# Performance work log

Measured on AMD Instinct MI355X. Metric: run time of the kernel, lower is better.

The kernel has to match this reference:

```python
import jax, jax.numpy as jnp
import numpy as np

EPS = 1e-5

def _bn(x, g, b):
    # BatchNorm2d in training mode: batch stats over (N,H,W), biased variance
    m = x.mean(axis=(0, 2, 3), keepdims=True)
    v = x.var(axis=(0, 2, 3), keepdims=True)
    return g[None, :, None, None] * (x - m) * jax.lax.rsqrt(v + EPS) + b[None, :, None, None]

def _conv(x, w, b, stride, pad):
    y = jax.lax.conv_general_dilated(x, w, (stride, stride), [(pad, pad), (pad, pad)],
                                     dimension_numbers=('NCHW', 'OIHW', 'NCHW'))
    return y + b[None, :, None, None]

def _convT(x, w, b):
    # torch ConvTranspose2d(k=4, s=2, p=1); w is torch layout (C_in, C_out, kH, kW)
    wt = jnp.flip(w, axis=(2, 3)).transpose(1, 0, 2, 3)  # -> OIHW
    y = jax.lax.conv_general_dilated(x, wt, (1, 1), [(2, 2), (2, 2)], lhs_dilation=(2, 2),
                                     dimension_numbers=('NCHW', 'OIHW', 'NCHW'))
    return y + b[None, :, None, None]

def setup_inputs() -> dict:
    key = jax.random.key(0)
    ks = jax.random.split(key, 20)
    K, C = 512, 64
    r = lambda k, sh, s=0.05: (jax.random.normal(k, sh, dtype=jnp.float32) * s)
    return {
        'x': jax.random.uniform(ks[0], (256, 1, 128, 128), dtype=jnp.float32),
        'enc_w1': r(ks[1], (16, 1, 4, 4)), 'enc_b1': r(ks[2], (16,)),
        'bn1_g': jnp.ones((16,), jnp.float32), 'bn1_b': jnp.zeros((16,), jnp.float32),
        'enc_w2': r(ks[3], (32, 16, 4, 4)), 'enc_b2': r(ks[4], (32,)),
        'bn2_g': jnp.ones((32,), jnp.float32), 'bn2_b': jnp.zeros((32,), jnp.float32),
        'enc_w3': r(ks[5], (64, 32, 1, 1)), 'enc_b3': r(ks[6], (64,)),
        'bn3_g': jnp.ones((64,), jnp.float32), 'bn3_b': jnp.zeros((64,), jnp.float32),
        'emb': jax.random.normal(ks[7], (K, C), dtype=jnp.float32) / K,
        'dec_w1': r(ks[8], (32, 64, 1, 1)), 'dec_b1': r(ks[9], (32,)),
        'bn4_g': jnp.ones((32,), jnp.float32), 'bn4_b': jnp.zeros((32,), jnp.float32),
        'dec_w2': r(ks[10], (32, 16, 4, 4)), 'dec_b2': r(ks[11], (16,)),  # ConvT torch layout (in,out,kh,kw)
        'bn5_g': jnp.ones((16,), jnp.float32), 'bn5_b': jnp.zeros((16,), jnp.float32),
        'dec_w3': r(ks[12], (16, 1, 4, 4)), 'dec_b3': r(ks[13], (1,)),
    }

def reference(x, enc_w1, enc_b1, bn1_g, bn1_b, enc_w2, enc_b2, bn2_g, bn2_b,
              enc_w3, enc_b3, bn3_g, bn3_b, emb,
              dec_w1, dec_b1, bn4_g, bn4_b, dec_w2, dec_b2, bn5_g, bn5_b,
              dec_w3, dec_b3):
    # ---- encoder ----
    h = jax.nn.relu(_bn(_conv(x, enc_w1, enc_b1, 2, 1), bn1_g, bn1_b))
    h = jax.nn.relu(_bn(_conv(h, enc_w2, enc_b2, 2, 1), bn2_g, bn2_b))
    z_e_x = _bn(_conv(h, enc_w3, enc_b3, 1, 0), bn3_g, bn3_b)  # [N,64,H/4,W/4]
    # ---- VQ: nearest codebook entry by squared L2 ----
    z = z_e_x.transpose(0, 2, 3, 1)  # NHWC
    dists = ((z * z).sum(-1, keepdims=True)
             - 2.0 * jnp.einsum('nhwc,kc->nhwk', z, emb)
             + (emb * emb).sum(-1))  # [N,H,W,K]
    latents = jnp.argmin(dists, axis=-1)
    z_q_x = emb[latents].transpose(0, 3, 1, 2)  # [N,64,H/4,W/4]
    # ---- decoder ----
    d = jax.nn.relu(_bn(_conv(z_q_x, dec_w1, dec_b1, 1, 0), bn4_g, bn4_b))
    d = jax.nn.relu(_bn(_convT(d, dec_w2, dec_b2), bn5_g, bn5_b))
    x_tilde = jax.nn.sigmoid(_convT(d, dec_w3, dec_b3))
    return (x_tilde, z_e_x, z_q_x)
```

## Files before the change

kernel.cpp:

```cpp
#include <hip/hip_runtime.h>

__device__ inline double wave_red(double v) {
#pragma unroll
  for (int off = 32; off > 0; off >>= 1) v += __shfl_down(v, off, 64);
  return v;
}
__device__ inline double block_red(double v, double* lds) {
  double w = wave_red(v);
  int lane = threadIdx.x & 63, wid = threadIdx.x >> 6;
  if (lane == 0) lds[wid] = w;
  __syncthreads();
  double r = 0.0;
  if (threadIdx.x == 0) r = (lds[0] + lds[1]) + (lds[2] + lds[3]);
  __syncthreads();
  return r;
}

__global__ __launch_bounds__(256) void conv1_k(const float* __restrict__ x, const float* __restrict__ w,
                                               const float* __restrict__ bias, float* __restrict__ y) {
  int t = blockIdx.x * 256 + threadIdx.x;
  int n = t >> 12, oh = (t >> 6) & 63, ow = t & 63;
  const float* xb = x + n * 16384;
  int ih0 = 2 * oh - 1, iw0 = 2 * ow - 1;
  float patch[16];
#pragma unroll
  for (int kh = 0; kh < 4; ++kh) {
    int ih = ih0 + kh;
    bool vh = (unsigned)ih < 128u;
#pragma unroll
    for (int kw = 0; kw < 4; ++kw) {
      int iw = iw0 + kw;
      patch[kh * 4 + kw] = (vh && (unsigned)iw < 128u) ? xb[ih * 128 + iw] : 0.f;
    }
  }
  float* yb = y + n * 65536 + oh * 64 + ow;
#pragma unroll
  for (int c = 0; c < 16; ++c) {
    float acc = 0.f;
#pragma unroll
    for (int q = 0; q < 16; ++q) acc = fmaf(patch[q], w[c * 16 + q], acc);
    yb[c * 4096] = __fadd_rn(acc, bias[c]);
  }
}

__global__ __launch_bounds__(256) void statsA_k(const float* __restrict__ y, double* __restrict__ ps,
                                                double* __restrict__ pq, int hwlog, int C, int M, int SPLIT) {
  int c = blockIdx.x, s = blockIdx.y;
  int HWm = (1 << hwlog) - 1;
  double sum = 0.0, sq = 0.0;
  for (int i = s * 256 + threadIdx.x; i < M; i += SPLIT * 256) {
    int n = i >> hwlog, hw = i & HWm;
    double v = (double)y[(size_t)n * (C << hwlog) + (c << hwlog) + hw];
    sum += v;
    sq = fma(v, v, sq);
  }
  __shared__ double lds[4];
  double S = block_red(sum, lds);
  double Q = block_red(sq, lds);
  if (threadIdx.x == 0) { ps[c * SPLIT + s] = S; pq[c * SPLIT + s] = Q; }
}

__global__ void finB_k(const double* __restrict__ ps, const double* __restrict__ pq,
                       float* __restrict__ ss, int C, int SPLIT, double invM) {
  int c = threadIdx.x;
  if (c >= C) return;
  double S = 0.0, Q = 0.0;
  for (int i = 0; i < SPLIT; ++i) { S += ps[c * SPLIT + i]; Q += pq[c * SPLIT + i]; }
  double mean = S * invM;
  float m32 = (float)mean;
  double v = Q * invM - 2.0 * (double)m32 * mean + (double)m32 * (double)m32;
  float v32 = (float)v;
  ss[c] = m32;
  ss[C + c] = 1.0f / sqrtf(__fadd_rn(v32, 1e-5f));
}

__global__ __launch_bounds__(256) void conv2_k(const float* __restrict__ y1, const float* __restrict__ ss,
                                               const float* __restrict__ w, const float* __restrict__ bias,
                                               float* __restrict__ y2) {
  int t = blockIdx.x * 256 + threadIdx.x;
  int n = t >> 10, oh = (t >> 5) & 31, ow = t & 31;
  const float* xb = y1 + n * 65536;
  int ih0 = 2 * oh - 1, iw0 = 2 * ow - 1;
  float acc[32];
#pragma unroll
  for (int co = 0; co < 32; ++co) acc[co] = 0.f;
  for (int ci = 0; ci < 16; ++ci) {
    float m = ss[ci], r = ss[16 + ci];
    const float* xc = xb + ci * 4096;
    float patch[16];
#pragma unroll
    for (int kh = 0; kh < 4; ++kh) {
      int ih = ih0 + kh;
      bool vh = (unsigned)ih < 64u;
#pragma unroll
      for (int kw = 0; kw < 4; ++kw) {
        int iw = iw0 + kw;
        float v = 0.f;
        if (vh && (unsigned)iw < 64u) v = fmaxf(__fmul_rn(__fsub_rn(xc[ih * 64 + iw], m), r), 0.f);
        patch[kh * 4 + kw] = v;
      }
    }
#pragma unroll
    for (int co = 0; co < 32; ++co) {
      const float* wc = w + (co * 16 + ci) * 16;
#pragma unroll
      for (int q = 0; q < 16; ++q) acc[co] = fmaf(patch[q], wc[q], acc[co]);
    }
  }
  float* yb = y2 + n * 32768 + oh * 32 + ow;
#pragma unroll
  for (int co = 0; co < 32; ++co) yb[co * 1024] = __fadd_rn(acc[co], bias[co]);
}

__global__ __launch_bounds__(256) void conv3_k(const float* __restrict__ y2, const float* __restrict__ ss,
                                               const float* __restrict__ w, const float* __restrict__ bias,
                                               float* __restrict__ y3) {
  int t = blockIdx.x * 256 + threadIdx.x;
  int n = t >> 10, hw = t & 1023;
  const float* xb = y2 + n * 32768 + hw;
  float h[32];
#pragma unroll
  for (int ci = 0; ci < 32; ++ci)
    h[ci] = fmaxf(__fmul_rn(__fsub_rn(xb[ci * 1024], ss[ci]), ss[32 + ci]), 0.f);
  float* yb = y3 + n * 65536 + hw;
  for (int c = 0; c < 64; ++c) {
    float acc = 0.f;
#pragma unroll
    for (int ci = 0; ci < 32; ++ci) acc = fmaf(h[ci], w[c * 32 + ci], acc);
    yb[c * 1024] = __fadd_rn(acc, bias[c]);
  }
}

__global__ void prepC_k(const float* __restrict__ emb, float* __restrict__ Ck) {
  int k = blockIdx.x * 64 + threadIdx.x;
  if (k >= 512) return;
  const float* e = emb + k * 64;
  float r8[8];
#pragma unroll
  for (int j = 0; j < 8; ++j) r8[j] = __fmul_rn(e[j], e[j]);
#pragma unroll
  for (int i = 8; i < 64; i += 8)
#pragma unroll
    for (int j = 0; j < 8; ++j) r8[j] = __fadd_rn(r8[j], __fmul_rn(e[i + j], e[i + j]));
  float a = __fadd_rn(__fadd_rn(r8[0], r8[1]), __fadd_rn(r8[2], r8[3]));
  float b = __fadd_rn(__fadd_rn(r8[4], r8[5]), __fadd_rn(r8[6], r8[7]));
  Ck[k] = __fadd_rn(a, b);
}

__global__ __launch_bounds__(256, 4) void vq4_k(const float* __restrict__ y3, const float* __restrict__ ss,
                                                const float* __restrict__ emb, const float* __restrict__ Ck,
                                                float* __restrict__ ze, float* __restrict__ zq) {
  int t = blockIdx.x * 256 + threadIdx.x;
  int n = t >> 10, hw = t & 1023;
  size_t base = (size_t)n * 65536 + hw;
  float z[64];
#pragma unroll
  for (int c = 0; c < 64; ++c) {
    float v = __fmul_rn(__fsub_rn(y3[base + (size_t)c * 1024], ss[c]), ss[64 + c]);
    z[c] = v;
    ze[base + (size_t)c * 1024] = v;
  }
  float r8[8];
#pragma unroll
  for (int j = 0; j < 8; ++j) r8[j] = __fmul_rn(z[j], z[j]);
#pragma unroll
  for (int i = 8; i < 64; i += 8)
#pragma unroll
    for (int j = 0; j < 8; ++j) r8[j] = __fadd_rn(r8[j], __fmul_rn(z[i + j], z[i + j]));
  float zz = __fadd_rn(__fadd_rn(__fadd_rn(r8[0], r8[1]), __fadd_rn(r8[2], r8[3])),
                       __fadd_rn(__fadd_rn(r8[4], r8[5]), __fadd_rn(r8[6], r8[7])));

  float best = 1e38f;
  int bi = 0;
  for (int k = 0; k < 512; k += 2) {
    const float* ea = emb + k * 64;
    const float* eb = ea + 64;
    float ga = 0.f, gb = 0.f;
#pragma unroll
    for (int c = 0; c < 64; ++c) {
      ga = __fadd_rn(ga, __fmul_rn(z[c], ea[c]));
      gb = __fadd_rn(gb, __fmul_rn(z[c], eb[c]));
    }
    float da = __fadd_rn(__fsub_rn(zz, __fmul_rn(2.f, ga)), Ck[k]);
    float db = __fadd_rn(__fsub_rn(zz, __fmul_rn(2.f, gb)), Ck[k + 1]);
    if (da < best) { best = da; bi = k; }
    if (db < best) { best = db; bi = k + 1; }
  }
  const float* ebi = emb + bi * 64;
#pragma unroll
  for (int c = 0; c < 64; ++c) zq[base + (size_t)c * 1024] = ebi[c];
}

__global__ __launch_bounds__(256) void dconv1_k(const float* __restrict__ zq, const float* __restrict__ w,
                                                const float* __restrict__ bias, float* __restrict__ y4) {
  int t = blockIdx.x * 256 + threadIdx.x;
  int n = t >> 10, hw = t & 1023;
  const float* xb = zq + (size_t)n * 65536 + hw;
  float acc[32];
#pragma unroll
  for (int co = 0; co < 32; ++co) acc[co] = 0.f;
  for (int ci = 0; ci < 64; ++ci) {
    float v = xb[(size_t)ci * 1024];
#pragma unroll
    for (int co = 0; co < 32; ++co) acc[co] = fmaf(v, w[co * 64 + ci], acc[co]);
  }
  float* yb = y4 + n * 32768 + hw;
#pragma unroll
  for (int co = 0; co < 32; ++co) yb[co * 1024] = __fadd_rn(acc[co], bias[co]);
}

__global__ __launch_bounds__(256) void convt5_k(const float* __restrict__ y4, const float* __restrict__ ss,
                                                const float* __restrict__ w, const float* __restrict__ bias,
                                                float* __restrict__ y5) {
  int t = blockIdx.x * 256 + threadIdx.x;
  int n = t >> 10, p = (t >> 5) & 31, q = t & 31;
  const float* xb = y4 + n * 32768;
  float acc[64];
#pragma unroll
  for (int i = 0; i < 64; ++i) acc[i] = 0.f;
  for (int ci = 0; ci < 32; ++ci) {
    float m = ss[ci], r = ss[32 + ci];
    const float* xc = xb + ci * 1024;
    float pt[9];
#pragma unroll
    for (int rr = 0; rr < 3; ++rr) {
      int ih = p - 1 + rr;
      bool vh = (unsigned)ih < 32u;
#pragma unroll
      for (int cc = 0; cc < 3; ++cc) {
        int iw = q - 1 + cc;
        float v = 0.f;
        if (vh && (unsigned)iw < 32u) v = fmaxf(__fmul_rn(__fsub_rn(xc[ih * 32 + iw], m), r), 0.f);
        pt[rr * 3 + cc] = v;
      }
    }
#pragma unroll
    for (int co = 0; co < 16; ++co) {
      const float* wb = w + (ci * 16 + co) * 16;
      float* a = acc + co * 4;
      a[0] = fmaf(pt[4], wb[5],  fmaf(pt[3], wb[7],  fmaf(pt[1], wb[13], fmaf(pt[0], wb[15], a[0]))));
      a[1] = fmaf(pt[5], wb[4],  fmaf(pt[4], wb[6],  fmaf(pt[2], wb[12], fmaf(pt[1], wb[14], a[1]))));
      a[2] = fmaf(pt[7], wb[1],  fmaf(pt[6], wb[3],  fmaf(pt[4], wb[9],  fmaf(pt[3], wb[11], a[2]))));
      a[3] = fmaf(pt[8], wb[0],  fmaf(pt[7], wb[2],  fmaf(pt[5], wb[8],  fmaf(pt[4], wb[10], a[3]))));
    }
  }
  float* yb = y5 + n * 65536;
  int r0 = (2 * p) * 64 + 2 * q;
#pragma unroll
  for (int co = 0; co < 16; ++co) {
    float b = bias[co];
    float* o = yb + co * 4096 + r0;
    *(float2*)(o)      = make_float2(__fadd_rn(acc[co * 4 + 0], b), __fadd_rn(acc[co * 4 + 1], b));
    *(float2*)(o + 64) = make_float2(__fadd_rn(acc[co * 4 + 2], b), __fadd_rn(acc[co * 4 + 3], b));
  }
}

__global__ __launch_bounds__(256) void convt6_k(const float* __restrict__ y5, const float* __restrict__ ss,
                                                const float* __restrict__ w, const float* __restrict__ b3,
                                                float* __restrict__ xt) {
  int t = blockIdx.x * 256 + threadIdx.x;
  int n = t >> 12, p = (t >> 6) & 63, q = t & 63;
  const float* xb = y5 + n * 65536;
  float a0 = 0.f, a1 = 0.f, a2 = 0.f, a3 = 0.f;
  for (int ci = 0; ci < 16; ++ci) {
    float m = ss[ci], r = ss[16 + ci];
    const float* xc = xb + ci * 4096;
    float pt[9];
#pragma unroll
    for (int rr = 0; rr < 3; ++rr) {
      int ih = p - 1 + rr;
      bool vh = (unsigned)ih < 64u;
#pragma unroll
      for (int cc = 0; cc < 3; ++cc) {
        int iw = q - 1 + cc;
        float v = 0.f;
        if (vh && (unsigned)iw < 64u) v = fmaxf(__fmul_rn(__fsub_rn(xc[ih * 64 + iw], m), r), 0.f);
        pt[rr * 3 + cc] = v;
      }
    }
    const float* wb = w + ci * 16;
    a0 = fmaf(pt[4], wb[5],  fmaf(pt[3], wb[7],  fmaf(pt[1], wb[13], fmaf(pt[0], wb[15], a0))));
    a1 = fmaf(pt[5], wb[4],  fmaf(pt[4], wb[6],  fmaf(pt[2], wb[12], fmaf(pt[1], wb[14], a1))));
    a2 = fmaf(pt[7], wb[1],  fmaf(pt[6], wb[3],  fmaf(pt[4], wb[9],  fmaf(pt[3], wb[11], a2))));
    a3 = fmaf(pt[8], wb[0],  fmaf(pt[7], wb[2],  fmaf(pt[5], wb[8],  fmaf(pt[4], wb[10], a3))));
  }
  float bb = b3[0];
  a0 = 1.f / __fadd_rn(1.f, expf(-__fadd_rn(a0, bb)));
  a1 = 1.f / __fadd_rn(1.f, expf(-__fadd_rn(a1, bb)));
  a2 = 1.f / __fadd_rn(1.f, expf(-__fadd_rn(a2, bb)));
  a3 = 1.f / __fadd_rn(1.f, expf(-__fadd_rn(a3, bb)));
  float* o = xt + n * 16384 + (2 * p) * 128 + 2 * q;
  *(float2*)o         = make_float2(a0, a1);
  *(float2*)(o + 128) = make_float2(a2, a3);
}

extern "C" void kernel_launch(void* const* d_in, const int* in_sizes, int n_in,
                              void* d_out, int out_size, void* d_ws, size_t ws_size,
                              hipStream_t stream) {
  const float* x      = (const float*)d_in[0];
  const float* enc_w1 = (const float*)d_in[1];
  const float* enc_b1 = (const float*)d_in[2];
  const float* enc_w2 = (const float*)d_in[5];
  const float* enc_b2 = (const float*)d_in[6];
  const float* enc_w3 = (const float*)d_in[9];
  const float* enc_b3 = (const float*)d_in[10];
  const float* emb    = (const float*)d_in[13];
  const float* dec_w1 = (const float*)d_in[14];
  const float* dec_b1 = (const float*)d_in[15];
  const float* dec_w2 = (const float*)d_in[18];
  const float* dec_b2 = (const float*)d_in[19];
  const float* dec_w3 = (const float*)d_in[22];
  const float* dec_b3 = (const float*)d_in[23];

  float* out = (float*)d_out;
  float* xt = out;
  float* ze = out + 4194304;
  float* zq = out + 20971520;

  char* W = (char*)d_ws;
  float* y1 = (float*)(W);
  float* y2 = (float*)(W + 67108864);
  float* y3 = (float*)(W);
  float* y4 = (float*)(W + 67108864);
  float* y5 = (float*)(W);
  char* P = W + 100663296;
  double* ps  = (double*)(P);
  double* pq  = (double*)(P + 32768);
  float* ss1  = (float*)(P + 65536);
  float* ss2  = ss1 + 128;
  float* ss3  = ss2 + 128;
  float* ss4  = ss3 + 128;
  float* ss5  = ss4 + 128;
  float* CkB  = ss5 + 128;

  hipLaunchKernelGGL(conv1_k, dim3(4096), dim3(256), 0, stream, x, enc_w1, enc_b1, y1);
  hipLaunchKernelGGL(statsA_k, dim3(16, 64), dim3(256), 0, stream, y1, ps, pq, 12, 16, 1048576, 64);
  hipLaunchKernelGGL(finB_k, dim3(1), dim3(64), 0, stream, ps, pq, ss1, 16, 64, 1.0 / 1048576.0);
  hipLaunchKernelGGL(conv2_k, dim3(1024), dim3(256), 0, stream, y1, ss1, enc_w2, enc_b2, y2);
  hipLaunchKernelGGL(statsA_k, dim3(32, 32), dim3(256), 0, stream, y2, ps, pq, 10, 32, 262144, 32);
  hipLaunchKernelGGL(finB_k, dim3(1), dim3(64), 0, stream, ps, pq, ss2, 32, 32, 1.0 / 262144.0);
  hipLaunchKernelGGL(conv3_k, dim3(1024), dim3(256), 0, stream, y2, ss2, enc_w3, enc_b3, y3);
  hipLaunchKernelGGL(statsA_k, dim3(64, 16), dim3(256), 0, stream, y3, ps, pq, 10, 64, 262144, 16);
  hipLaunchKernelGGL(finB_k, dim3(1), dim3(64), 0, stream, ps, pq, ss3, 64, 16, 1.0 / 262144.0);

  hipLaunchKernelGGL(prepC_k, dim3(8), dim3(64), 0, stream, emb, CkB);
  hipLaunchKernelGGL(vq4_k, dim3(1024), dim3(256), 0, stream, y3, ss3, emb, CkB, ze, zq);

  hipLaunchKernelGGL(dconv1_k, dim3(1024), dim3(256), 0, stream, zq, dec_w1, dec_b1, y4);
  hipLaunchKernelGGL(statsA_k, dim3(32, 32), dim3(256), 0, stream, y4, ps, pq, 10, 32, 262144, 32);
  hipLaunchKernelGGL(finB_k, dim3(1), dim3(64), 0, stream, ps, pq, ss4, 32, 32, 1.0 / 262144.0);
  hipLaunchKernelGGL(convt5_k, dim3(1024), dim3(256), 0, stream, y4, ss4, dec_w2, dec_b2, y5);
  hipLaunchKernelGGL(statsA_k, dim3(16, 64), dim3(256), 0, stream, y5, ps, pq, 12, 16, 1048576, 64);
  hipLaunchKernelGGL(finB_k, dim3(1), dim3(64), 0, stream, ps, pq, ss5, 16, 64, 1.0 / 1048576.0);
  hipLaunchKernelGGL(convt6_k, dim3(4096), dim3(256), 0, stream, y5, ss5, dec_w3, dec_b3, xt);
}
```

Measured before the change: 837.7 us.

## Two-pass VQ argmin: fast FMA screening with candidate list, exact rescoring

The VQ kernel now computes approximate distances with independent FMA chains over float4 codebook loads. Each thread keeps a per-thread LDS list of codes within a small threshold of its running minimum. Only those candidates are rescored with the original strictly ordered, round-to-nearest arithmetic to pick the exact argmin, falling back to a full exact scan when the list overflows. This targets the long serial dependent add chain of the exact distance loop, at the cost of extra LDS use and some branch divergence.

```diff
diff --git a/kernel.cpp b/kernel.cpp
--- a/kernel.cpp
+++ b/kernel.cpp
@@ -147,45 +147,116 @@
   Ck[k] = __fadd_rn(a, b);
 }
 
-__global__ __launch_bounds__(256, 4) void vq4_k(const float* __restrict__ y3, const float* __restrict__ ss,
-                                                const float* __restrict__ emb, const float* __restrict__ Ck,
-                                                float* __restrict__ ze, float* __restrict__ zq) {
+#define DEXACT(kk, dout)                                              \
+  {                                                                   \
+    const float4* e4_ = (const float4*)(emb + (kk) * 64);             \
+    float g_ = 0.f;                                                   \
+    _Pragma("unroll") for (int c4 = 0; c4 < 16; ++c4) {               \
+      float4 e_ = e4_[c4];                                            \
+      g_ = __fadd_rn(g_, __fmul_rn(za[2 * c4].x, e_.x));              \
+      g_ = __fadd_rn(g_, __fmul_rn(za[2 * c4].y, e_.y));              \
+      g_ = __fadd_rn(g_, __fmul_rn(za[2 * c4 + 1].x, e_.z));          \
+      g_ = __fadd_rn(g_, __fmul_rn(za[2 * c4 + 1].y, e_.w));          \
+    }                                                                 \
+    dout = __fadd_rn(__fsub_rn(zz, __fmul_rn(2.f, g_)), Ck[(kk)]);    \
+  }
+
+__global__ __launch_bounds__(256) void vq5_k(const float* __restrict__ y3, const float* __restrict__ ss,
+                                             const float* __restrict__ emb, const float* __restrict__ Ck,
+                                             float* __restrict__ ze, float* __restrict__ zq) {
+  __shared__ unsigned short lst[256 * 16];
   int t = blockIdx.x * 256 + threadIdx.x;
   int n = t >> 10, hw = t & 1023;
   size_t base = (size_t)n * 65536 + hw;
-  float z[64];
-#pragma unroll
-  for (int c = 0; c < 64; ++c) {
-    float v = __fmul_rn(__fsub_rn(y3[base + (size_t)c * 1024], ss[c]), ss[64 + c]);
-    z[c] = v;
-    ze[base + (size_t)c * 1024] = v;
-  }
+
+  float2 za[32];
+#pragma unroll
+  for (int j = 0; j < 32; ++j) {
+    float vx = __fmul_rn(__fsub_rn(y3[base + (size_t)(2 * j) * 1024], ss[2 * j]), ss[64 + 2 * j]);
+    float vy = __fmul_rn(__fsub_rn(y3[base + (size_t)(2 * j + 1) * 1024], ss[2 * j + 1]), ss[64 + 2 * j + 1]);
+    za[j] = make_float2(vx, vy);
+    ze[base + (size_t)(2 * j) * 1024] = vx;
+    ze[base + (size_t)(2 * j + 1) * 1024] = vy;
+  }
+#pragma unroll
+  for (int j = 0; j < 32; ++j) asm volatile("" : "+v"(za[j].x), "+v"(za[j].y));
+
   float r8[8];
 #pragma unroll
-  for (int j = 0; j < 8; ++j) r8[j] = __fmul_rn(z[j], z[j]);
+  for (int j = 0; j < 8; ++j) {
+    float zc = (j & 1) ? za[j >> 1].y : za[j >> 1].x;
+    r8[j] = __fmul_rn(zc, zc);
+  }
 #pragma unroll
   for (int i = 8; i < 64; i += 8)
 #pragma unroll
-    for (int j = 0; j < 8; ++j) r8[j] = __fadd_rn(r8[j], __fmul_rn(z[i + j], z[i + j]));
+    for (int j = 0; j < 8; ++j) {
+      float zc = ((i + j) & 1) ? za[(i + j) >> 1].y : za[(i + j) >> 1].x;
+      r8[j] = __fadd_rn(r8[j], __fmul_rn(zc, zc));
+    }
   float zz = __fadd_rn(__fadd_rn(__fadd_rn(r8[0], r8[1]), __fadd_rn(r8[2], r8[3])),
                        __fadd_rn(__fadd_rn(r8[4], r8[5]), __fadd_rn(r8[6], r8[7])));
 
+  const float T = 1e-4f;
+  float m1 = 1e38f;
+  int cnt = 0;
+  int lbase = threadIdx.x << 4;
+
+#define APPEND(df, kk)                                                   \
+  {                                                                      \
+    if ((df) <= m1 + T) {                                                \
+      if (cnt < 16) lst[lbase | cnt] = (unsigned short)(kk);             \
+      ++cnt;                                                             \
+    }                                                                    \
+    m1 = fminf(m1, (df));                                                \
+  }
+
+  for (int k = 0; k < 512; k += 4) {
+    const float4* e0 = (const float4*)(emb + k * 64);
+    float4 a0 = make_float4(0.f, 0.f, 0.f, 0.f);
+    float4 a1 = a0, a2 = a0, a3 = a0;
+#pragma unroll
+    for (int j = 0; j < 16; ++j) {
+      float2 zl = za[2 * j], zh = za[2 * j + 1];
+      float4 ea = e0[j], eb = e0[16 + j], ec = e0[32 + j], ed = e0[48 + j];
+      a0.x = fmaf(zl.x, ea.x, a0.x); a0.y = fmaf(zl.y, ea.y, a0.y);
+      a0.z = fmaf(zh.x, ea.z, a0.z); a0.w = fmaf(zh.y, ea.w, a0.w);
+      a1.x = fmaf(zl.x, eb.x, a1.x); a1.y = fmaf(zl.y, eb.y, a1.y);
+      a1.z = fmaf(zh.x, eb.z, a1.z); a1.w = fmaf(zh.y, eb.w, a1.w);
+      a2.x = fmaf(zl.x, ec.x, a2.x); a2.y = fmaf(zl.y, ec.y, a2.y);
+      a2.z = fmaf(zh.x, ec.z, a2.z); a2.w = fmaf(zh.y, ec.w, a2.w);
+      a3.x = fmaf(zl.x, ed.x, a3.x); a3.y = fmaf(zl.y, ed.y, a3.y);
+      a3.z = fmaf(zh.x, ed.z, a3.z); a3.w = fmaf(zh.y, ed.w, a3.w);
+    }
+    float g0 = (a0.x + a0.y) + (a0.z + a0.w);
+    float g1 = (a1.x + a1.y) + (a1.z + a1.w);
+    float g2 = (a2.x + a2.y) + (a2.z + a2.w);
+    float g3 = (a3.x + a3.y) + (a3.z + a3.w);
+    float d0 = fmaf(-2.f, g0, Ck[k]);
+    float d1 = fmaf(-2.f, g1, Ck[k + 1]);
+    float d2 = fmaf(-2.f, g2, Ck[k + 2]);
+    float d3 = fmaf(-2.f, g3, Ck[k + 3]);
+    APPEND(d0, k) APPEND(d1, k + 1) APPEND(d2, k + 2) APPEND(d3, k + 3)
+  }
+#undef APPEND
+
+  int bi = 0;
   float best = 1e38f;
-  int bi = 0;
-  for (int k = 0; k < 512; k += 2) {
-    const float* ea = emb + k * 64;
-    const float* eb = ea + 64;
-    float ga = 0.f, gb = 0.f;
-#pragma unroll
-    for (int c = 0; c < 64; ++c) {
-      ga = __fadd_rn(ga, __fmul_rn(z[c], ea[c]));
-      gb = __fadd_rn(gb, __fmul_rn(z[c], eb[c]));
-    }
-    float da = __fadd_rn(__fsub_rn(zz, __fmul_rn(2.f, ga)), Ck[k]);
-    float db = __fadd_rn(__fsub_rn(zz, __fmul_rn(2.f, gb)), Ck[k + 1]);
-    if (da < best) { best = da; bi = k; }
-    if (db < best) { best = db; bi = k + 1; }
-  }
+  if (cnt > 16) {
+    for (int k = 0; k < 512; ++k) {
+      float d;
+      DEXACT(k, d)
+      if (d < best) { best = d; bi = k; }
+    }
+  } else {
+    for (int j = 0; j < cnt; ++j) {
+      int k = lst[lbase | j];
+      float d;
+      DEXACT(k, d)
+      if (d < best) { best = d; bi = k; }
+    }
+  }
+
   const float* ebi = emb + bi * 64;
 #pragma unroll
   for (int c = 0; c < 64; ++c) zq[base + (size_t)c * 1024] = ebi[c];
@@ -344,7 +415,7 @@
   hipLaunchKernelGGL(finB_k, dim3(1), dim3(64), 0, stream, ps, pq, ss3, 64, 16, 1.0 / 262144.0);
 
   hipLaunchKernelGGL(prepC_k, dim3(8), dim3(64), 0, stream, emb, CkB);
-  hipLaunchKernelGGL(vq4_k, dim3(1024), dim3(256), 0, stream, y3, ss3, emb, CkB, ze, zq);
+  hipLaunchKernelGGL(vq5_k, dim3(1024), dim3(256), 0, stream, y3, ss3, emb, CkB, ze, zq);
 
   hipLaunchKernelGGL(dconv1_k, dim3(1024), dim3(256), 0, stream, zq, dec_w1, dec_b1, y4);
   hipLaunchKernelGGL(statsA_k, dim3(32, 32), dim3(256), 0, stream, y4, ps, pq, 10, 32, 262144, 32);
```

Result: slower. 1.221 ms (+45.8%).
